# Performance work log

Measured on AMD Instinct MI355X. Metric: run time of the kernel, lower is better.

The kernel has to match this reference:

```python
import jax, jax.numpy as jnp
import numpy as np
from jax import lax

DIM = 64           # LHMSA dim
C3 = 3 * DIM       # high-band channels
HEADS = C3 // 32   # 6
WS = 8             # window size
SHIFT = 4          # shift size
EPS = 1e-6


def _ln_chw(x, w, b):
    # channel-last layer norm applied to BCHW input over C
    xt = x.transpose(0, 2, 3, 1)
    mu = xt.mean(-1, keepdims=True)
    var = ((xt - mu) ** 2).mean(-1, keepdims=True)
    y = (xt - mu) / jnp.sqrt(var + EPS) * w + b
    return y.transpose(0, 3, 1, 2)


def _conv1x1(x, w):
    # w: (out_c, in_c), no bias
    return jnp.einsum('bchw,oc->bohw', x, w)


def _dwconv3(x, w):
    # depthwise 3x3, w: (C,1,3,3)
    C = x.shape[1]
    return lax.conv_general_dilated(x, w, (1, 1), ((1, 1), (1, 1)),
                                    dimension_numbers=('NCHW', 'OIHW', 'NCHW'),
                                    feature_group_count=C)


def _gelu(x):
    return jax.nn.gelu(x, approximate=False)


def _dwt(x):
    x01 = x[:, :, 0::2, :] * 0.5
    x02 = x[:, :, 1::2, :] * 0.5
    x1 = x01[:, :, :, 0::2]; x2 = x02[:, :, :, 0::2]
    x3 = x01[:, :, :, 1::2]; x4 = x02[:, :, :, 1::2]
    ll = x1 + x2 + x3 + x4
    high = jnp.concatenate([-x1 - x2 + x3 + x4,
                            -x1 + x2 - x3 + x4,
                            x1 - x2 - x3 + x4], axis=1)
    return ll, high


def _iwt(ll, high):
    B, C, H, W = ll.shape
    hl, lh, hh = jnp.split(high, 3, axis=1)
    x1 = (ll - hl - lh + hh) * 0.5
    x2 = (ll - hl + lh - hh) * 0.5
    x3 = (ll + hl - lh - hh) * 0.5
    x4 = (ll + hl + lh + hh) * 0.5
    even = jnp.stack([x1, x3], axis=-1).reshape(B, C, H, 2 * W)  # rows 0::2
    odd = jnp.stack([x2, x4], axis=-1).reshape(B, C, H, 2 * W)   # rows 1::2
    return jnp.stack([even, odd], axis=-2).reshape(B, C, 2 * H, 2 * W)


def _swin_mhsa(x, qkv_w, qkv_b, proj_w, proj_b, rpb_table, rpi):
    # x: (B, C3, H, W); H,W divisible by WS -> no padding path
    B, C, H, W = x.shape
    dh = C // HEADS
    scale = dh ** (-0.5)
    xh = x.transpose(0, 2, 3, 1)                           # BHWC
    xh = jnp.roll(xh, (-SHIFT, -SHIFT), axis=(1, 2))
    nh, nw = H // WS, W // WS
    xw = xh.reshape(B, nh, WS, nw, WS, C).transpose(0, 1, 3, 2, 4, 5)
    xw = xw.reshape(B * nh * nw, WS * WS, C)               # (nW, N, C)
    qkv = xw @ qkv_w.T + qkv_b                             # (nW, N, 3C)
    qkv = qkv.reshape(-1, WS * WS, 3, HEADS, dh).transpose(2, 0, 3, 1, 4)
    q, k, v = qkv[0], qkv[1], qkv[2]                       # (nW, h, N, dh)
    attn = jnp.einsum('whnd,whmd->whnm', q, k) * scale
    bias = rpb_table[rpi.reshape(-1)].reshape(WS * WS, WS * WS, HEADS)
    attn = jax.nn.softmax(attn + bias.transpose(2, 0, 1)[None], axis=-1)
    out = jnp.einsum('whnm,whmd->whnd', attn, v)
    out = out.transpose(0, 2, 1, 3).reshape(-1, WS * WS, C)
    out = out.reshape(B, nh, nw, WS, WS, C).transpose(0, 1, 3, 2, 4, 5)
    out = out.reshape(B, H, W, C)
    out = jnp.roll(out, (SHIFT, SHIFT), axis=(1, 2))
    out = out @ proj_w.T + proj_b
    return out.transpose(0, 3, 1, 2)


def _rel_pos_index():
    coords = np.stack(np.meshgrid(np.arange(WS), np.arange(WS), indexing='ij'))
    cf = coords.reshape(2, -1)
    rel = (cf[:, :, None] - cf[:, None, :]).transpose(1, 2, 0).astype(np.int64)
    rel[:, :, 0] += WS - 1
    rel[:, :, 1] += WS - 1
    rel[:, :, 0] *= 2 * WS - 1
    return rel.sum(-1)


def setup_inputs() -> dict:
    key = jax.random.key(0)
    ks = jax.random.split(key, 12)
    B, H, W = 2, 512, 512
    x = jax.random.normal(ks[0], (B, DIM, H, W), jnp.float32)
    s = 0.02
    inp = {
        'x': x,
        'norm_w': jnp.ones((C3,), jnp.float32),
        'norm_b': jnp.zeros((C3,), jnp.float32),
        'qkv_w': jax.random.normal(ks[1], (3 * C3, C3), jnp.float32) * s,
        'qkv_b': jnp.zeros((3 * C3,), jnp.float32),
        'proj_w': jax.random.normal(ks[2], (C3, C3), jnp.float32) * s,
        'proj_b': jnp.zeros((C3,), jnp.float32),
        'rpb_table': jax.random.normal(ks[3], ((2 * WS - 1) ** 2, HEADS), jnp.float32) * s,
        'aux_dw_w': jax.random.normal(ks[4], (DIM, 1, 3, 3), jnp.float32) * 0.1,
        'aux_pw_w': jax.random.normal(ks[5], (DIM, DIM), jnp.float32) * s,
        'cg1_w': jax.random.normal(ks[6], (C3 * 3 // 12, DIM), jnp.float32) * s,
        'cg2_w': jax.random.normal(ks[7], (C3, C3 * 3 // 12), jnp.float32) * s,
        'po_w': jax.random.normal(ks[8], (DIM, DIM), jnp.float32) * s,
        'gamma_main': jnp.full((1,), 1e-4, jnp.float32),
        'gamma_aux': jnp.full((1,), 0.5, jnp.float32),
        'gamma_cross': jnp.full((1,), 1e-5, jnp.float32),
        'rel_pos_index': jnp.asarray(_rel_pos_index(), jnp.int32),
    }
    return inp


def reference(x, norm_w, norm_b, qkv_w, qkv_b, proj_w, proj_b, rpb_table,
              aux_dw_w, aux_pw_w, cg1_w, cg2_w, po_w,
              gamma_main, gamma_aux, gamma_cross, rel_pos_index):
    ll, high = _dwt(x)
    high_norm = _ln_chw(high, norm_w, norm_b)
    refined_high = high + gamma_main * _swin_mhsa(high_norm, qkv_w, qkv_b,
                                                  proj_w, proj_b, rpb_table,
                                                  rel_pos_index)
    refined_ll = ll + gamma_aux * _conv1x1(_gelu(_dwconv3(ll, aux_dw_w)), aux_pw_w)
    gap = ll.mean((2, 3), keepdims=True)
    cross = jax.nn.sigmoid(_conv1x1(_gelu(_conv1x1(gap, cg1_w)), cg2_w))
    refined_high = refined_high * (1.0 + gamma_cross * (cross - 0.5) * 2.0)
    out = _iwt(refined_ll, refined_high)
    return _conv1x1(out - x, po_w)
```

## Files before the change

### kernel.cpp

```cpp
#include <hip/hip_runtime.h>
#include <hip/hip_bf16.h>
#include <math.h>

typedef __hip_bfloat16 bf16;
typedef short s8v __attribute__((ext_vector_type(8)));
typedef float f4v __attribute__((ext_vector_type(4)));
#define MFMA16(a,b,c) __builtin_amdgcn_mfma_f32_16x16x32_bf16(a,b,c,0,0,0)

#define B2   2
#define C64  64
#define C3   192
#define HEADS 6
#define NWIN 2048

#define P_NORMW 0
#define P_NORMB 192
#define P_QKVW  384
#define P_QKVB  110976
#define P_PROJW 111552
#define P_PROJB 148416
#define P_RPB   148608
#define P_AUXDW 149958
#define P_AUXPW 150534
#define P_CG1   154630
#define P_CG2   157702
#define P_PO    166918
#define P_GM    171014
#define P_GA    171015
#define P_GC    171016

#define WS_FLAG   0
#define WS_PARAMS 256
#define WS_GAP    684544
#define WS_AMUL   685568
#define WS_CVAL   687616
#define WS_TSTAT  689664
#define WS_LL     1738240
#define WS_DLLW   18515456
#define WS_WOUT   35292672
#define WS_HRAW   85624320
#define WS_WQKV   135955968
#define WS_WPROJ  136177152
#define WS_WPW    136250880
#define WS_WPO    136259072
#define WS_S12    136267264
#define WS_BIAS6  136271872

template<bool ISF>
__device__ __forceinline__ float LD(const void* p, long i){
  if constexpr (ISF) return ((const float*)p)[i];
  else return __bfloat162float(((const bf16*)p)[i]);
}
template<bool ISF>
__device__ __forceinline__ float2 LD2(const void* p, long i){
  if constexpr (ISF) return *(const float2*)((const float*)p + i);
  else {
    const ushort2 u = *(const ushort2*)((const bf16*)p + i);
    float2 r; r.x = __uint_as_float(((unsigned)u.x) << 16);
    r.y = __uint_as_float(((unsigned)u.y) << 16);
    return r;
  }
}
template<bool ISF>
__device__ __forceinline__ void ST(void* p, long i, float v){
  if constexpr (ISF) ((float*)p)[i] = v;
  else ((bf16*)p)[i] = __float2bfloat16(v);
}
__device__ __forceinline__ float gelu_f(float x){
  return 0.5f * x * (1.f + erff(x * 0.70710678118654752f));
}
__device__ __forceinline__ float bfu(unsigned short u){
  return __uint_as_float(((unsigned)u) << 16);
}
__device__ __forceinline__ unsigned pk2(float a, float b){
  return (unsigned)__bfloat16_as_ushort(__float2bfloat16(a)) |
         ((unsigned)__bfloat16_as_ushort(__float2bfloat16(b)) << 16);
}
__device__ __forceinline__ uint4 pk8(const float* v){
  uint4 r;
  r.x = pk2(v[0], v[1]); r.y = pk2(v[2], v[3]);
  r.z = pk2(v[4], v[5]); r.w = pk2(v[6], v[7]);
  return r;
}
__device__ __forceinline__ void gld16(const void* g, void* l){
  __builtin_amdgcn_global_load_lds(
      (const __attribute__((address_space(1))) void*)g,
      (__attribute__((address_space(3))) void*)l, 16, 0, 0);
}

__global__ __launch_bounds__(256) void detect_kernel(const void* x, int* flag){
  __shared__ int wildcnt;
  if (threadIdx.x == 0) wildcnt = 0;
  __syncthreads();
  const unsigned short* u = (const unsigned short*)x;
  int wild = 0;
  for (int i = threadIdx.x; i < 2048; i += 256){
    unsigned int v = ((unsigned int)u[i]) << 16;
    float f = __uint_as_float(v);
    float a = fabsf(f);
    if (!(a < 1e8f) || (a > 0.f && a < 1e-8f)) wild++;
  }
  atomicAdd(&wildcnt, wild);
  __syncthreads();
  if (threadIdx.x == 0) *flag = (wildcnt > 100) ? 1 : 0;
}

struct PP { const void* src[15]; float* dst[15]; int n[15]; };
__global__ __launch_bounds__(256) void convert_params(PP pp, const int* flag){
  const bool isf = (*flag) != 0;
  const int gid = blockIdx.x*256 + threadIdx.x;
  const int gsz = gridDim.x*256;
#pragma unroll
  for (int q = 0; q < 15; q++){
    const int n = pp.n[q];
    const void* s = pp.src[q];
    float* d = pp.dst[q];
    for (int i = gid; i < n; i += gsz)
      d[i] = isf ? ((const float*)s)[i] : __bfloat162float(((const bf16*)s)[i]);
  }
}

__global__ __launch_bounds__(256) void kw_convert(const float* pf, const int* rpi,
                                                  bf16* wqkvF, bf16* wproj,
                                                  bf16* wpw, bf16* wpo, float* bias6T){
  const int i = blockIdx.x*256 + threadIdx.x;
  if (i < 110592){
    const int c = i % 192;
    wqkvF[i] = __float2bfloat16(pf[P_QKVW + i] * pf[P_NORMW + c]);
  } else if (i < 147456)  wproj[i-110592] = __float2bfloat16(pf[P_PROJW + (i-110592)]);
  else if (i < 151552)    wpw[i-147456]   = __float2bfloat16(pf[P_AUXPW + (i-147456)]);
  else if (i < 155648)    wpo[i-151552]   = __float2bfloat16(pf[P_PO + (i-151552)]);
  else if (i < 180224){
    const int j = i - 155648;
    const int hh = j >> 12, nm = j & 4095;
    const int row = nm >> 6, col = nm & 63;
    bias6T[hh*4096 + col*64 + row] = pf[P_RPB + rpi[nm]*6 + hh];
  }
}

__global__ __launch_bounds__(256) void k0d_s12(const float* pf, float2* s12p){
  const int o = blockIdx.x*16 + (threadIdx.x >> 4);
  const int lane = threadIdx.x & 15;
  if (o >= 576) return;
  float s1 = 0.f, s2 = 0.f;
  for (int c = lane; c < 192; c += 16){
    const float w = pf[P_QKVW + o*192 + c];
    s1 += w * pf[P_NORMW + c];
    s2 += w * pf[P_NORMB + c];
  }
  s1 += __shfl_xor(s1,1,16); s1 += __shfl_xor(s1,2,16);
  s1 += __shfl_xor(s1,4,16); s1 += __shfl_xor(s1,8,16);
  s2 += __shfl_xor(s2,1,16); s2 += __shfl_xor(s2,2,16);
  s2 += __shfl_xor(s2,4,16); s2 += __shfl_xor(s2,8,16);
  if (lane == 0){
    float2 v; v.x = s1; v.y = s2 + pf[P_QKVB + o];
    s12p[o] = v;
  }
}

template<bool ISF>
__device__ void k1f_body(const void* xv, bf16* llb, bf16* hraw, float2* tstat){
  const int wid = blockIdx.x;
  const int b  = wid >> 10;
  const int wh = (wid >> 5) & 31;
  const int ww = wid & 31;
  const int tid = threadIdx.x;
  const int tk = tid >> 2, l4 = tid & 3;
  const int wi = tk >> 3, wj = tk & 7;
  const int h2 = (wh*8 + wi + 4) & 255;
  const int w2 = (ww*8 + wj + 4) & 255;
  const long pixbase = ((long)(2*h2) << 9) + 2*w2;
  const long llpix = ((long)h2 << 8) + w2;
  float raw0[16], raw1[16], raw2[16];
  float sum = 0.f, sumsq = 0.f;
#pragma unroll
  for (int cc = 0; cc < 16; ++cc){
    const int c = l4*16 + cc;
    const long base = ((long)(b*64 + c) << 18) + pixbase;
    const float2 t0 = LD2<ISF>(xv, base);
    const float2 t1 = LD2<ISF>(xv, base + 512);
    const float a = t0.x, cr = t0.y, bb = t1.x, dd = t1.y;
    llb[((long)(b*64 + c) << 16) + llpix] = __float2bfloat16(0.5f*(a + bb + cr + dd));
    const float h0 = 0.5f*(-a - bb + cr + dd);
    const float h1 = 0.5f*(-a + bb - cr + dd);
    const float hh = 0.5f*( a - bb - cr + dd);
    raw0[cc] = h0; raw1[cc] = h1; raw2[cc] = hh;
    sum += h0 + h1 + hh;
    sumsq += h0*h0 + h1*h1 + hh*hh;
  }
  const long hb = ((long)wid*64 + tk)*192 + l4*16;
  *(uint4*)(hraw + hb)       = pk8(raw0);
  *(uint4*)(hraw + hb + 8)   = pk8(raw0 + 8);
  *(uint4*)(hraw + hb + 64)  = pk8(raw1);
  *(uint4*)(hraw + hb + 72)  = pk8(raw1 + 8);
  *(uint4*)(hraw + hb + 128) = pk8(raw2);
  *(uint4*)(hraw + hb + 136) = pk8(raw2 + 8);
  sum   += __shfl_xor(sum,1,4);   sum   += __shfl_xor(sum,2,4);
  sumsq += __shfl_xor(sumsq,1,4); sumsq += __shfl_xor(sumsq,2,4);
  if (l4 == 0){
    const float mean = sum * (1.f/192.f);
    float var = sumsq * (1.f/192.f) - mean*mean;
    var = fmaxf(var, 0.f);
    const float rstd = rsqrtf(var + 1e-6f);
    float2 st; st.x = rstd; st.y = mean * rstd;
    tstat[wid*64 + tk] = st;
  }
}
__global__ __launch_bounds__(256,4) void k1f_dwt(const void* xv, bf16* llb, bf16* hraw,
                                                 float2* tstat, const int* flag){
  if (*flag) k1f_body<true>(xv, llb, hraw, tstat);
  else       k1f_body<false>(xv, llb, hraw, tstat);
}

__global__ __launch_bounds__(256) void k2_gap(const bf16* llb, float* gap){
  const int bc = blockIdx.x;
  const uint4* p = (const uint4*)(llb + ((long)bc << 16));
  float s = 0.f;
  for (int i = threadIdx.x; i < 8192; i += 256){
    const uint4 v = p[i];
    s += __uint_as_float(v.x << 16) + __uint_as_float(v.x & 0xffff0000u);
    s += __uint_as_float(v.y << 16) + __uint_as_float(v.y & 0xffff0000u);
    s += __uint_as_float(v.z << 16) + __uint_as_float(v.z & 0xffff0000u);
    s += __uint_as_float(v.w << 16) + __uint_as_float(v.w & 0xffff0000u);
  }
  __shared__ float red[256];
  red[threadIdx.x] = s; __syncthreads();
  for (int st = 128; st > 0; st >>= 1){
    if (threadIdx.x < st) red[threadIdx.x] += red[threadIdx.x + st];
    __syncthreads();
  }
  if (threadIdx.x == 0) gap[bc] = red[0] * (1.f / 65536.f);
}

__global__ __launch_bounds__(256) void k3_cross(const float* pf, const float* gap,
                                                float* amul, float* cval){
  __shared__ float t1[B2][48];
  __shared__ float g[B2][64];
  const int tid = threadIdx.x;
  if (tid < 128) g[tid >> 6][tid & 63] = gap[tid];
  __syncthreads();
  if (tid < 96){
    const int b = tid / 48, j = tid % 48;
    float s = 0.f;
    const float* w = pf + P_CG1 + j * 64;
    for (int c = 0; c < 64; ++c) s += w[c] * g[b][c];
    t1[b][j] = gelu_f(s);
  }
  __syncthreads();
  const float gm = pf[P_GM], gc = pf[P_GC];
  for (int o = tid; o < B2 * C3; o += 256){
    const int b = o / C3, ch = o % C3;
    float s = 0.f;
    const float* w = pf + P_CG2 + ch * 48;
    for (int j = 0; j < 48; ++j) s += w[j] * t1[b][j];
    const float cr = 1.f / (1.f + expf(-s));
    const float c = gc * (cr - 0.5f) * 2.f;
    cval[o] = c;
    amul[o] = gm * (1.f + c);
  }
}

__global__ __launch_bounds__(256,6) void k6f_aux(const bf16* llb, const float* pf,
                                                 const bf16* wpw, bf16* dllw){
  __shared__ __align__(16) char sm6[24576];
  bf16* tile = (bf16*)sm6;
  bf16* t    = (bf16*)(sm6 + 15360);
  const int blk = blockIdx.x;
  const int b = blk >> 10, ti = (blk >> 5) & 31, tj = blk & 31;
  const int tid = threadIdx.x;
  const int y0 = ti*8 - 1;
  const int x0 = tj*8 - 2;

  for (int e = tid; e < 7680; e += 256){
    const int col = e % 12;
    const int rc  = e / 12;
    const int row = rc % 10, ch = rc / 10;
    const int x = x0 + col, y = y0 + row;
    bf16 v = __float2bfloat16(0.f);
    if ((unsigned)x < 256u && (unsigned)y < 256u)
      v = llb[((long)(b*64 + ch) << 16) + ((long)y << 8) + x];
    tile[rc*12 + col] = v;
  }
  __syncthreads();

  {
    const int tok = tid & 63, cgrp = tid >> 6;
    const int iy = tok >> 3, ix = tok & 7;
#pragma unroll
    for (int cc = 0; cc < 16; ++cc){
      const int c = cgrp*16 + cc;
      const float* wk = pf + P_AUXDW + c*9;
      float s = 0.f;
#pragma unroll
      for (int ky = 0; ky < 3; ++ky)
#pragma unroll
        for (int kx = 0; kx < 3; ++kx)
          s += wk[ky*3 + kx] * __bfloat162float(tile[(c*10 + iy + ky)*12 + ix + 1 + kx]);
      t[tok*72 + c] = __float2bfloat16(gelu_f(s));
    }
  }
  __syncthreads();

  const int wv = tid >> 6, l = tid & 63, lr = l & 15, lg = l >> 4;
  const f4v fz = {0.f,0.f,0.f,0.f};
  f4v acc[4];
#pragma unroll
  for (int nt = 0; nt < 4; ++nt) acc[nt] = fz;
#pragma unroll
  for (int ks = 0; ks < 2; ++ks){
    const s8v a = *(const s8v*)(t + (wv*16+lr)*72 + ks*32 + lg*8);
#pragma unroll
    for (int nt = 0; nt < 4; ++nt){
      const s8v bfr = *(const s8v*)(wpw + (nt*16+lr)*64 + ks*32 + lg*8);
      acc[nt] = MFMA16(a, bfr, acc[nt]);
    }
  }
  const float ga = pf[P_GA];
#pragma unroll
  for (int i = 0; i < 4; ++i){
    const int p = wv*16 + lg*4 + i;
    const int y = ti*8 + (p >> 3), x = tj*8 + (p & 7);
    const int sy = (y - 4) & 255, sx = (x - 4) & 255;
    const int wid = b*1024 + (sy >> 3)*32 + (sx >> 3);
    const int tok2 = (sy & 7)*8 + (sx & 7);
    const long ob = ((long)wid*64 + tok2)*64;
#pragma unroll
    for (int nt = 0; nt < 4; ++nt)
      dllw[ob + nt*16 + lr] = __float2bfloat16(ga * acc[nt][i]);
  }
}

__global__ __launch_bounds__(512,4) void k4_attn(const bf16* hraw, const float2* tstat,
                                                 const bf16* wqkvF, const float2* s12p,
                                                 const float* bias6T, bf16* wout){
  __shared__ __align__(16) char sm[63488];
  bf16* bstage = (bf16*)sm;
  const int g = blockIdx.x;
  const int xcd = g & 7, slot = g >> 3;
  const int pair = (slot/6)*8 + xcd;
  const int h    = slot - (slot/6)*6;
  const int tid = threadIdx.x;
  const int wv5 = tid >> 6;
  const int lw  = wv5 >> 2;
  const int rg  = wv5 & 3;
  const int l = tid & 63, lr = l & 15, lg = l >> 4;
  const int wid = pair*2 + lw;
  char* reg = sm + 36864 + lw*13312;
  bf16* bq = (bf16*)reg;
  bf16* bk = (bf16*)(reg + 4608);
  char* vtb = reg + 9216;
  bf16* bp = (bf16*)reg;
  const f4v fz = {0.f,0.f,0.f,0.f};
  const float scale = 0.17677669529663687f;
  const bf16* at = hraw + (long)wid * 12288;

#pragma unroll
  for (int pass = 0; pass < 5; ++pass){
    if (pass*512 + wv5*64 < 2304){
      const int idx = pass*512 + tid;
      const int rl  = idx / 24;
      const int off = (idx - rl*24) * 16;
      const int soff = off ^ ((rl & 7) << 4);
      const int grow = (rl >> 5)*192 + h*32 + (rl & 31);
      gld16(wqkvF + grow*192 + (soff >> 1),
            (char*)bstage + (pass*512 + wv5*64)*16);
    }
  }
  s8v aA[6];
#pragma unroll
  for (int ks = 0; ks < 6; ++ks)
    aA[ks] = *(const s8v*)(at + (rg*16+lr)*192 + ks*32 + lg*8);
  float2 st4[4];
#pragma unroll
  for (int i = 0; i < 4; ++i)
    st4[i] = tstat[wid*64 + rg*16 + lg*4 + i];
  __syncthreads();

  f4v acc[6];
#pragma unroll
  for (int nt = 0; nt < 6; ++nt) acc[nt] = fz;
#pragma unroll
  for (int ks = 0; ks < 6; ++ks){
    const int kb = (ks*32 + lg*8) * 2;
#pragma unroll
    for (int nt = 0; nt < 6; ++nt){
      const int row = nt*16 + lr;
      const s8v bfr = *(const s8v*)((const char*)bstage + row*384 + (kb ^ ((row&7)<<4)));
      acc[nt] = MFMA16(aA[ks], bfr, acc[nt]);
    }
  }
#pragma unroll
  for (int nt = 0; nt < 6; ++nt){
    const int ol = nt*16 + lr;
    const int p = ol >> 5, c = ol & 31;
    const int ocol = p*192 + h*32 + c;
    const float2 sp = s12p[ocol];
#pragma unroll
    for (int i = 0; i < 4; ++i){
      const int row = rg*16 + lg*4 + i;
      const float v = st4[i].x*acc[nt][i] - st4[i].y*sp.x + sp.y;
      if (p == 0)      bq[row*36 + c] = __float2bfloat16(v*scale);
      else if (p == 1) bk[row*36 + c] = __float2bfloat16(v);
      else             *(bf16*)(vtb + ((c*128 + row*2) ^ ((c&7)<<4))) = __float2bfloat16(v);
    }
  }
  __syncthreads();

  f4v sacc[4];
  {
    const s8v a = *(const s8v*)(bq + (rg*16+lr)*36 + lg*8);
#pragma unroll
    for (int nt = 0; nt < 4; ++nt){
      const s8v bfr = *(const s8v*)(bk + (nt*16+lr)*36 + lg*8);
      sacc[nt] = MFMA16(a, bfr, fz);
    }
  }
  f4v bld[4];
#pragma unroll
  for (int nt = 0; nt < 4; ++nt)
    bld[nt] = *(const f4v*)(bias6T + h*4096 + (nt*16+lr)*64 + rg*16 + lg*4);
  float pvv[4][4];
  float inv4[4];
#pragma unroll
  for (int i = 0; i < 4; ++i){
    float s = 0.f;
#pragma unroll
    for (int nt = 0; nt < 4; ++nt){
      const float e = __expf(sacc[nt][i] + bld[nt][i]);
      pvv[i][nt] = e;
      s += e;
    }
    s += __shfl_xor(s, 1, 16);
    s += __shfl_xor(s, 2, 16);
    s += __shfl_xor(s, 4, 16);
    s += __shfl_xor(s, 8, 16);
    inv4[i] = 1.f/s;
  }
  __syncthreads();

#pragma unroll
  for (int i = 0; i < 4; ++i){
    const int row = rg*16 + lg*4 + i;
#pragma unroll
    for (int nt = 0; nt < 4; ++nt)
      bp[row*72 + nt*16 + lr] = __float2bfloat16(pvv[i][nt]);
  }
  f4v oacc[2] = {fz, fz};
#pragma unroll
  for (int ks2 = 0; ks2 < 2; ++ks2){
    const s8v a = *(const s8v*)(bp + (rg*16+lr)*72 + ks2*32 + lg*8);
#pragma unroll
    for (int nn = 0; nn < 2; ++nn){
      const int d = nn*16 + lr;
      const s8v bfr = *(const s8v*)(vtb + ((d*128 + (ks2*32+lg*8)*2) ^ ((d&7)<<4)));
      oacc[nn] = MFMA16(a, bfr, oacc[nn]);
    }
  }
#pragma unroll
  for (int nn = 0; nn < 2; ++nn)
#pragma unroll
    for (int i = 0; i < 4; ++i){
      const int row = rg*16 + lg*4 + i;
      wout[((long)wid*64 + row)*192 + h*32 + nn*16 + lr] =
        __float2bfloat16(oacc[nn][i] * inv4[i]);
    }
}

__global__ __launch_bounds__(256,5) void k5_proj(bf16* wout, const bf16* hraw,
                                                 const bf16* wproj, const float* pf,
                                                 const float* amul, const float* cval){
  __shared__ __align__(16) bf16 bufC[64*192];
  const int wid = blockIdx.x;
  const int b  = wid >> 10;
  const int tid = threadIdx.x;
  const int wv = tid >> 6, l = tid & 63, lr = l & 15, lg = l >> 4;

  {
    const bf16* hsrc = hraw + (long)wid * 12288;
#pragma unroll
    for (int pass = 0; pass < 6; ++pass){
      const int idx = pass*256 + tid;
      const int row = idx / 24;
      const int off = (idx % 24) * 16;
      const int soff = off ^ ((row & 7) << 4);
      gld16(hsrc + row*192 + (soff >> 1),
            (char*)bufC + (pass*256 + wv*64)*16);
    }
  }

  const f4v fz = {0.f,0.f,0.f,0.f};
  const bf16* at = wout + (long)wid * 12288;

  f4v acc[3][4];
#pragma unroll
  for (int nt = 0; nt < 3; ++nt)
#pragma unroll
    for (int mt = 0; mt < 4; ++mt) acc[nt][mt] = fz;
#pragma unroll
  for (int ks = 0; ks < 6; ++ks){
    const int k0 = ks*32;
    s8v a[4];
#pragma unroll
    for (int mt = 0; mt < 4; ++mt)
      a[mt] = *(const s8v*)(at + (mt*16+lr)*192 + k0 + lg*8);
#pragma unroll
    for (int nt = 0; nt < 3; ++nt){
      const int ocol = (wv*3+nt)*16 + lr;
      const s8v bfr = *(const s8v*)(wproj + ocol*192 + k0 + lg*8);
#pragma unroll
      for (int mt = 0; mt < 4; ++mt) acc[nt][mt] = MFMA16(a[mt], bfr, acc[nt][mt]);
    }
  }
  __syncthreads();
#pragma unroll
  for (int nt = 0; nt < 3; ++nt){
    const int col = (wv*3+nt)*16 + lr;
    const int bc = b*192 + col;
    const float am = amul[bc], cv = cval[bc], pb = pf[P_PROJB + col];
#pragma unroll
    for (int mt = 0; mt < 4; ++mt)
#pragma unroll
      for (int i = 0; i < 4; ++i){
        const int row = mt*16 + lg*4 + i;
        const float hv = __bfloat162float(
          *(const bf16*)((const char*)bufC + row*384 + ((col*2) ^ ((row&7)<<4))));
        wout[(long)wid*12288 + row*192 + col] =
          __float2bfloat16(am*(acc[nt][mt][i] + pb) + cv*hv);
      }
  }
}

template<bool ISF>
__device__ void k7_body(const bf16* dvalw, const bf16* dllw, const bf16* wpo,
                        void* out, char* yp){
  const int blk = blockIdx.x;
  const int b = blk >> 10, hh = (blk >> 1) & 511, half = blk & 1;
  const int h2 = hh >> 1, posH = hh & 1;
  const int th = (h2 + 252) & 255;
  const int wh = th >> 3, wi = th & 7;
  const int tid = threadIdx.x;
  const int j = tid & 7;
#pragma unroll
  for (int pass = 0; pass < 8; ++pass){
    const int p = pass*32 + (tid >> 3);
    const int ww2 = half*256 + p;
    const int w2 = ww2 >> 1, posW = ww2 & 1;
    const int tw = (w2 + 252) & 255;
    const int ww = tw >> 3, wj = tw & 7;
    const int wid = b*1024 + wh*32 + ww;
    const int tok = wi*8 + wj;
    const long dvb = ((long)wid*64 + tok)*192 + j*8;
    const s8v hl8 = *(const s8v*)(dvalw + dvb);
    const s8v lh8 = *(const s8v*)(dvalw + dvb + 64);
    const s8v hh8 = *(const s8v*)(dvalw + dvb + 128);
    const s8v dl8 = *(const s8v*)(dllw + ((long)wid*64 + tok)*64 + j*8);
    const float s1 = posW ? 0.5f : -0.5f;
    const float s2 = posH ? 0.5f : -0.5f;
    const float s3 = posW == posH ? 0.5f : -0.5f;
    float e[8];
#pragma unroll
    for (int q = 0; q < 8; ++q)
      e[q] = 0.5f*bfu((unsigned short)dl8[q]) + s1*bfu((unsigned short)hl8[q])
           + s2*bfu((unsigned short)lh8[q]) + s3*bfu((unsigned short)hh8[q]);
    *(uint4*)(yp + ((p*128 + j*16) ^ ((p&7)<<4))) = pk8(e);
  }
  __syncthreads();
  const int wv = tid >> 6, l = tid & 63, lr = l & 15, lg = l >> 4;
  const f4v fz = {0.f,0.f,0.f,0.f};
  f4v acc[4][4];
#pragma unroll
  for (int mt = 0; mt < 4; ++mt)
#pragma unroll
    for (int nt = 0; nt < 4; ++nt) acc[mt][nt] = fz;
#pragma unroll
  for (int ks = 0; ks < 2; ++ks){
    const int k0 = ks*32;
    s8v a[4];
#pragma unroll
    for (int mt = 0; mt < 4; ++mt)
      a[mt] = *(const s8v*)(wpo + (mt*16+lr)*64 + k0 + lg*8);
#pragma unroll
    for (int nt = 0; nt < 4; ++nt){
      const int prow = wv*64 + nt*16 + lr;
      const s8v bfr = *(const s8v*)(yp + ((prow*128 + (k0+lg*8)*2) ^ ((prow&7)<<4)));
#pragma unroll
      for (int mt = 0; mt < 4; ++mt) acc[mt][nt] = MFMA16(a[mt], bfr, acc[mt][nt]);
    }
  }
  const int px0 = half*256 + wv*64;
#pragma unroll
  for (int mt = 0; mt < 4; ++mt)
#pragma unroll
    for (int nt = 0; nt < 4; ++nt)
#pragma unroll
      for (int i = 0; i < 4; ++i){
        const int c = mt*16 + lg*4 + i;
        const long ob = ((long)(b*64 + c)*512 + hh)*512 + px0 + nt*16 + lr;
        ST<ISF>(out, ob, acc[mt][nt][i]);
      }
}
__global__ __launch_bounds__(256,4) void k7_out(const bf16* dvalw, const bf16* dllw,
                                                const bf16* wpo, void* out, const int* flag){
  __shared__ __align__(16) char yp[32768];
  if (*flag) k7_body<true>(dvalw, dllw, wpo, out, yp);
  else       k7_body<false>(dvalw, dllw, wpo, out, yp);
}

extern "C" void kernel_launch(void* const* d_in, const int* in_sizes, int n_in,
                              void* d_out, int out_size, void* d_ws, size_t ws_size,
                              hipStream_t stream){
  char* ws = (char*)d_ws;
  int*   flag = (int*)(ws + WS_FLAG);
  float* pf   = (float*)(ws + WS_PARAMS);
  float* gap  = (float*)(ws + WS_GAP);
  float* amul = (float*)(ws + WS_AMUL);
  float* cval = (float*)(ws + WS_CVAL);
  float2* tstat=(float2*)(ws + WS_TSTAT);
  bf16*  llb  = (bf16*)(ws + WS_LL);
  bf16*  dllw = (bf16*)(ws + WS_DLLW);
  bf16*  wout = (bf16*)(ws + WS_WOUT);
  bf16*  hraw = (bf16*)(ws + WS_HRAW);
  bf16*  wqkvF= (bf16*)(ws + WS_WQKV);
  bf16*  wproj= (bf16*)(ws + WS_WPROJ);
  bf16*  wpw  = (bf16*)(ws + WS_WPW);
  bf16*  wpo  = (bf16*)(ws + WS_WPO);
  float2* s12p= (float2*)(ws + WS_S12);
  float* bias6= (float*)(ws + WS_BIAS6);
  const int* rpi = (const int*)d_in[16];

  detect_kernel<<<1, 256, 0, stream>>>(d_in[0], flag);

  PP pp;
  const int pidx[15] = {1,2,3,4,5,6,7,8,9,10,11,12,13,14,15};
  const int poff[15] = {P_NORMW,P_NORMB,P_QKVW,P_QKVB,P_PROJW,P_PROJB,P_RPB,
                        P_AUXDW,P_AUXPW,P_CG1,P_CG2,P_PO,P_GM,P_GA,P_GC};
  for (int q = 0; q < 15; q++){
    pp.src[q] = d_in[pidx[q]];
    pp.dst[q] = pf + poff[q];
    pp.n[q]   = in_sizes[pidx[q]];
  }
  convert_params<<<128, 256, 0, stream>>>(pp, flag);
  kw_convert<<<704, 256, 0, stream>>>(pf, rpi, wqkvF, wproj, wpw, wpo, bias6);
  k0d_s12  <<<36,  256, 0, stream>>>(pf, s12p);

  k1f_dwt<<<NWIN, 256, 0, stream>>>(d_in[0], llb, hraw, tstat, flag);
  k2_gap <<<128,  256, 0, stream>>>(llb, gap);
  k3_cross<<<1,   256, 0, stream>>>(pf, gap, amul, cval);
  k6f_aux<<<NWIN, 256, 0, stream>>>(llb, pf, wpw, dllw);
  k4_attn<<<NWIN/2*6, 512, 0, stream>>>(hraw, tstat, wqkvF, s12p, bias6, wout);
  k5_proj<<<NWIN, 256, 0, stream>>>(wout, hraw, wproj, pf, amul, cval);
  k7_out <<<2048, 256, 0, stream>>>(wout, dllw, wpo, d_out, flag);
}
```

Measured before the change: 423.9 us.

## Merge attention, aux conv and GAP into one heterogeneous launch; widen DWT loads

Three independent kernels (window attention, the low-band aux depthwise/pointwise branch, and the global average pool) are merged into a single launch whose blocks branch on their index. The aim is to cut launch gaps and tail idle time so the small kernels fill the attention kernel's tail. The aux branch now packs two tiles per 512-thread block and the GAP uses 512 threads. Separately, the DWT kernel processes two tokens per thread with 4-wide loads and paired ll stores. Mixing workloads ties all blocks to the attention kernel's shared memory size and register budget, which may lower occupancy for the lighter paths.

```diff
diff --git a/kernel.cpp b/kernel.cpp
--- a/kernel.cpp
+++ b/kernel.cpp
@@ -47,17 +47,18 @@
 #define WS_BIAS6  136271872
 
 template<bool ISF>
-__device__ __forceinline__ float LD(const void* p, long i){
-  if constexpr (ISF) return ((const float*)p)[i];
-  else return __bfloat162float(((const bf16*)p)[i]);
+__device__ __forceinline__ float bfu_(unsigned short u){
+  return __uint_as_float(((unsigned)u) << 16);
+}
+__device__ __forceinline__ float bfu(unsigned short u){
+  return __uint_as_float(((unsigned)u) << 16);
 }
 template<bool ISF>
-__device__ __forceinline__ float2 LD2(const void* p, long i){
-  if constexpr (ISF) return *(const float2*)((const float*)p + i);
+__device__ __forceinline__ float4 LD4(const void* p, long i){
+  if constexpr (ISF) return *(const float4*)((const float*)p + i);
   else {
-    const ushort2 u = *(const ushort2*)((const bf16*)p + i);
-    float2 r; r.x = __uint_as_float(((unsigned)u.x) << 16);
-    r.y = __uint_as_float(((unsigned)u.y) << 16);
+    const ushort4 u = *(const ushort4*)((const bf16*)p + i);
+    float4 r; r.x = bfu(u.x); r.y = bfu(u.y); r.z = bfu(u.z); r.w = bfu(u.w);
     return r;
   }
 }
@@ -68,9 +69,6 @@
 }
 __device__ __forceinline__ float gelu_f(float x){
   return 0.5f * x * (1.f + erff(x * 0.70710678118654752f));
-}
-__device__ __forceinline__ float bfu(unsigned short u){
-  return __uint_as_float(((unsigned)u) << 16);
 }
 __device__ __forceinline__ unsigned pk2(float a, float b){
   return (unsigned)__bfloat16_as_ushort(__float2bfloat16(a)) |
@@ -165,71 +163,64 @@
   const int wh = (wid >> 5) & 31;
   const int ww = wid & 31;
   const int tid = threadIdx.x;
-  const int tk = tid >> 2, l4 = tid & 3;
-  const int wi = tk >> 3, wj = tk & 7;
+  const int tp = tid >> 3, l8 = tid & 7;
+  const int t0 = tp*2;
+  const int wi = t0 >> 3, wj0 = t0 & 7;
   const int h2 = (wh*8 + wi + 4) & 255;
-  const int w2 = (ww*8 + wj + 4) & 255;
-  const long pixbase = ((long)(2*h2) << 9) + 2*w2;
-  const long llpix = ((long)h2 << 8) + w2;
-  float raw0[16], raw1[16], raw2[16];
-  float sum = 0.f, sumsq = 0.f;
-#pragma unroll
-  for (int cc = 0; cc < 16; ++cc){
-    const int c = l4*16 + cc;
-    const long base = ((long)(b*64 + c) << 18) + pixbase;
-    const float2 t0 = LD2<ISF>(xv, base);
-    const float2 t1 = LD2<ISF>(xv, base + 512);
-    const float a = t0.x, cr = t0.y, bb = t1.x, dd = t1.y;
-    llb[((long)(b*64 + c) << 16) + llpix] = __float2bfloat16(0.5f*(a + bb + cr + dd));
-    const float h0 = 0.5f*(-a - bb + cr + dd);
-    const float h1 = 0.5f*(-a + bb - cr + dd);
-    const float hh = 0.5f*( a - bb - cr + dd);
-    raw0[cc] = h0; raw1[cc] = h1; raw2[cc] = hh;
-    sum += h0 + h1 + hh;
-    sumsq += h0*h0 + h1*h1 + hh*hh;
-  }
-  const long hb = ((long)wid*64 + tk)*192 + l4*16;
-  *(uint4*)(hraw + hb)       = pk8(raw0);
-  *(uint4*)(hraw + hb + 8)   = pk8(raw0 + 8);
-  *(uint4*)(hraw + hb + 64)  = pk8(raw1);
-  *(uint4*)(hraw + hb + 72)  = pk8(raw1 + 8);
-  *(uint4*)(hraw + hb + 128) = pk8(raw2);
-  *(uint4*)(hraw + hb + 136) = pk8(raw2 + 8);
-  sum   += __shfl_xor(sum,1,4);   sum   += __shfl_xor(sum,2,4);
-  sumsq += __shfl_xor(sumsq,1,4); sumsq += __shfl_xor(sumsq,2,4);
-  if (l4 == 0){
-    const float mean = sum * (1.f/192.f);
-    float var = sumsq * (1.f/192.f) - mean*mean;
-    var = fmaxf(var, 0.f);
-    const float rstd = rsqrtf(var + 1e-6f);
+  const int w2 = (ww*8 + wj0 + 4) & 255;
+  const long rowbase = ((long)(2*h2) << 9) + 2*w2;
+  float r0[3][8], r1[3][8];
+  float s0 = 0.f, q0 = 0.f, s1 = 0.f, q1 = 0.f;
+#pragma unroll
+  for (int cc = 0; cc < 8; ++cc){
+    const int c = l8*8 + cc;
+    const long base = ((long)(b*64 + c) << 18) + rowbase;
+    const float4 ta = LD4<ISF>(xv, base);
+    const float4 tb = LD4<ISF>(xv, base + 512);
+    float a = ta.x, cr = ta.y, bb = tb.x, dd = tb.y;
+    const float ll0 = 0.5f*(a + bb + cr + dd);
+    const float h00 = 0.5f*(-a - bb + cr + dd);
+    const float h10 = 0.5f*(-a + bb - cr + dd);
+    const float h20 = 0.5f*( a - bb - cr + dd);
+    r0[0][cc] = h00; r0[1][cc] = h10; r0[2][cc] = h20;
+    s0 += h00 + h10 + h20; q0 += h00*h00 + h10*h10 + h20*h20;
+    a = ta.z; cr = ta.w; bb = tb.z; dd = tb.w;
+    const float ll1 = 0.5f*(a + bb + cr + dd);
+    const float h01 = 0.5f*(-a - bb + cr + dd);
+    const float h11 = 0.5f*(-a + bb - cr + dd);
+    const float h21 = 0.5f*( a - bb - cr + dd);
+    r1[0][cc] = h01; r1[1][cc] = h11; r1[2][cc] = h21;
+    s1 += h01 + h11 + h21; q1 += h01*h01 + h11*h11 + h21*h21;
+    *(unsigned*)(llb + ((long)(b*64 + c) << 16) + ((long)h2 << 8) + w2) = pk2(ll0, ll1);
+  }
+  const long hb = ((long)wid*64 + t0)*192 + l8*8;
+  *(uint4*)(hraw + hb)            = pk8(r0[0]);
+  *(uint4*)(hraw + hb + 64)       = pk8(r0[1]);
+  *(uint4*)(hraw + hb + 128)      = pk8(r0[2]);
+  *(uint4*)(hraw + hb + 192)      = pk8(r1[0]);
+  *(uint4*)(hraw + hb + 192 + 64) = pk8(r1[1]);
+  *(uint4*)(hraw + hb + 192 +128) = pk8(r1[2]);
+  s0 += __shfl_xor(s0,1,8); s0 += __shfl_xor(s0,2,8); s0 += __shfl_xor(s0,4,8);
+  q0 += __shfl_xor(q0,1,8); q0 += __shfl_xor(q0,2,8); q0 += __shfl_xor(q0,4,8);
+  s1 += __shfl_xor(s1,1,8); s1 += __shfl_xor(s1,2,8); s1 += __shfl_xor(s1,4,8);
+  q1 += __shfl_xor(q1,1,8); q1 += __shfl_xor(q1,2,8); q1 += __shfl_xor(q1,4,8);
+  if (l8 == 0){
+    float mean = s0 * (1.f/192.f);
+    float var = fmaxf(q0 * (1.f/192.f) - mean*mean, 0.f);
+    float rstd = rsqrtf(var + 1e-6f);
     float2 st; st.x = rstd; st.y = mean * rstd;
-    tstat[wid*64 + tk] = st;
+    tstat[wid*64 + t0] = st;
+    mean = s1 * (1.f/192.f);
+    var = fmaxf(q1 * (1.f/192.f) - mean*mean, 0.f);
+    rstd = rsqrtf(var + 1e-6f);
+    st.x = rstd; st.y = mean * rstd;
+    tstat[wid*64 + t0 + 1] = st;
   }
 }
 __global__ __launch_bounds__(256,4) void k1f_dwt(const void* xv, bf16* llb, bf16* hraw,
                                                  float2* tstat, const int* flag){
   if (*flag) k1f_body<true>(xv, llb, hraw, tstat);
   else       k1f_body<false>(xv, llb, hraw, tstat);
-}
-
-__global__ __launch_bounds__(256) void k2_gap(const bf16* llb, float* gap){
-  const int bc = blockIdx.x;
-  const uint4* p = (const uint4*)(llb + ((long)bc << 16));
-  float s = 0.f;
-  for (int i = threadIdx.x; i < 8192; i += 256){
-    const uint4 v = p[i];
-    s += __uint_as_float(v.x << 16) + __uint_as_float(v.x & 0xffff0000u);
-    s += __uint_as_float(v.y << 16) + __uint_as_float(v.y & 0xffff0000u);
-    s += __uint_as_float(v.z << 16) + __uint_as_float(v.z & 0xffff0000u);
-    s += __uint_as_float(v.w << 16) + __uint_as_float(v.w & 0xffff0000u);
-  }
-  __shared__ float red[256];
-  red[threadIdx.x] = s; __syncthreads();
-  for (int st = 128; st > 0; st >>= 1){
-    if (threadIdx.x < st) red[threadIdx.x] += red[threadIdx.x + st];
-    __syncthreads();
-  }
-  if (threadIdx.x == 0) gap[bc] = red[0] * (1.f / 65536.f);
 }
 
 __global__ __launch_bounds__(256) void k3_cross(const float* pf, const float* gap,
@@ -260,82 +251,11 @@
   }
 }
 
-__global__ __launch_bounds__(256,6) void k6f_aux(const bf16* llb, const float* pf,
-                                                 const bf16* wpw, bf16* dllw){
-  __shared__ __align__(16) char sm6[24576];
-  bf16* tile = (bf16*)sm6;
-  bf16* t    = (bf16*)(sm6 + 15360);
-  const int blk = blockIdx.x;
-  const int b = blk >> 10, ti = (blk >> 5) & 31, tj = blk & 31;
-  const int tid = threadIdx.x;
-  const int y0 = ti*8 - 1;
-  const int x0 = tj*8 - 2;
-
-  for (int e = tid; e < 7680; e += 256){
-    const int col = e % 12;
-    const int rc  = e / 12;
-    const int row = rc % 10, ch = rc / 10;
-    const int x = x0 + col, y = y0 + row;
-    bf16 v = __float2bfloat16(0.f);
-    if ((unsigned)x < 256u && (unsigned)y < 256u)
-      v = llb[((long)(b*64 + ch) << 16) + ((long)y << 8) + x];
-    tile[rc*12 + col] = v;
-  }
-  __syncthreads();
-
-  {
-    const int tok = tid & 63, cgrp = tid >> 6;
-    const int iy = tok >> 3, ix = tok & 7;
-#pragma unroll
-    for (int cc = 0; cc < 16; ++cc){
-      const int c = cgrp*16 + cc;
-      const float* wk = pf + P_AUXDW + c*9;
-      float s = 0.f;
-#pragma unroll
-      for (int ky = 0; ky < 3; ++ky)
-#pragma unroll
-        for (int kx = 0; kx < 3; ++kx)
-          s += wk[ky*3 + kx] * __bfloat162float(tile[(c*10 + iy + ky)*12 + ix + 1 + kx]);
-      t[tok*72 + c] = __float2bfloat16(gelu_f(s));
-    }
-  }
-  __syncthreads();
-
-  const int wv = tid >> 6, l = tid & 63, lr = l & 15, lg = l >> 4;
-  const f4v fz = {0.f,0.f,0.f,0.f};
-  f4v acc[4];
-#pragma unroll
-  for (int nt = 0; nt < 4; ++nt) acc[nt] = fz;
-#pragma unroll
-  for (int ks = 0; ks < 2; ++ks){
-    const s8v a = *(const s8v*)(t + (wv*16+lr)*72 + ks*32 + lg*8);
-#pragma unroll
-    for (int nt = 0; nt < 4; ++nt){
-      const s8v bfr = *(const s8v*)(wpw + (nt*16+lr)*64 + ks*32 + lg*8);
-      acc[nt] = MFMA16(a, bfr, acc[nt]);
-    }
-  }
-  const float ga = pf[P_GA];
-#pragma unroll
-  for (int i = 0; i < 4; ++i){
-    const int p = wv*16 + lg*4 + i;
-    const int y = ti*8 + (p >> 3), x = tj*8 + (p & 7);
-    const int sy = (y - 4) & 255, sx = (x - 4) & 255;
-    const int wid = b*1024 + (sy >> 3)*32 + (sx >> 3);
-    const int tok2 = (sy & 7)*8 + (sx & 7);
-    const long ob = ((long)wid*64 + tok2)*64;
-#pragma unroll
-    for (int nt = 0; nt < 4; ++nt)
-      dllw[ob + nt*16 + lr] = __float2bfloat16(ga * acc[nt][i]);
-  }
-}
-
-__global__ __launch_bounds__(512,4) void k4_attn(const bf16* hraw, const float2* tstat,
-                                                 const bf16* wqkvF, const float2* s12p,
-                                                 const float* bias6T, bf16* wout){
-  __shared__ __align__(16) char sm[63488];
+
+__device__ void k4_body(char* sm, int g, const bf16* hraw, const float2* tstat,
+                        const bf16* wqkvF, const float2* s12p, const float* bias6T,
+                        bf16* wout){
   bf16* bstage = (bf16*)sm;
-  const int g = blockIdx.x;
   const int xcd = g & 7, slot = g >> 3;
   const int pair = (slot/6)*8 + xcd;
   const int h    = slot - (slot/6)*6;
@@ -464,6 +384,110 @@
       wout[((long)wid*64 + row)*192 + h*32 + nn*16 + lr] =
         __float2bfloat16(oacc[nn][i] * inv4[i]);
     }
+}
+
+__device__ void k6f_body(char* smb, int blk6, const bf16* llb, const float* pf,
+                         const bf16* wpw, bf16* dllw){
+  const int tid = threadIdx.x;
+  const int sub = tid >> 8;
+  const int t2 = tid & 255;
+  char* sm6 = smb + sub*24576;
+  bf16* tile = (bf16*)sm6;
+  bf16* t    = (bf16*)(sm6 + 15360);
+  const int tl = blk6*2 + sub;
+  const int b = tl >> 10, ti = (tl >> 5) & 31, tj = tl & 31;
+  const int y0 = ti*8 - 1;
+  const int x0 = tj*8 - 2;
+
+  for (int e = t2; e < 7680; e += 256){
+    const int col = e % 12;
+    const int rc  = e / 12;
+    const int row = rc % 10, ch = rc / 10;
+    const int x = x0 + col, y = y0 + row;
+    bf16 v = __float2bfloat16(0.f);
+    if ((unsigned)x < 256u && (unsigned)y < 256u)
+      v = llb[((long)(b*64 + ch) << 16) + ((long)y << 8) + x];
+    tile[rc*12 + col] = v;
+  }
+  __syncthreads();
+
+  {
+    const int tok = t2 & 63, cgrp = t2 >> 6;
+    const int iy = tok >> 3, ix = tok & 7;
+#pragma unroll
+    for (int cc = 0; cc < 16; ++cc){
+      const int c = cgrp*16 + cc;
+      const float* wk = pf + P_AUXDW + c*9;
+      float s = 0.f;
+#pragma unroll
+      for (int ky = 0; ky < 3; ++ky)
+#pragma unroll
+        for (int kx = 0; kx < 3; ++kx)
+          s += wk[ky*3 + kx] * __bfloat162float(tile[(c*10 + iy + ky)*12 + ix + 1 + kx]);
+      t[tok*72 + c] = __float2bfloat16(gelu_f(s));
+    }
+  }
+  __syncthreads();
+
+  const int wv = t2 >> 6, l = t2 & 63, lr = l & 15, lg = l >> 4;
+  const f4v fz = {0.f,0.f,0.f,0.f};
+  f4v acc[4];
+#pragma unroll
+  for (int nt = 0; nt < 4; ++nt) acc[nt] = fz;
+#pragma unroll
+  for (int ks = 0; ks < 2; ++ks){
+    const s8v a = *(const s8v*)(t + (wv*16+lr)*72 + ks*32 + lg*8);
+#pragma unroll
+    for (int nt = 0; nt < 4; ++nt){
+      const s8v bfr = *(const s8v*)(wpw + (nt*16+lr)*64 + ks*32 + lg*8);
+      acc[nt] = MFMA16(a, bfr, acc[nt]);
+    }
+  }
+  const float ga = pf[P_GA];
+#pragma unroll
+  for (int i = 0; i < 4; ++i){
+    const int p = wv*16 + lg*4 + i;
+    const int y = ti*8 + (p >> 3), x = tj*8 + (p & 7);
+    const int sy = (y - 4) & 255, sx = (x - 4) & 255;
+    const int wd = b*1024 + (sy >> 3)*32 + (sx >> 3);
+    const int tok2 = (sy & 7)*8 + (sx & 7);
+    const long ob = ((long)wd*64 + tok2)*64;
+#pragma unroll
+    for (int nt = 0; nt < 4; ++nt)
+      dllw[ob + nt*16 + lr] = __float2bfloat16(ga * acc[nt][i]);
+  }
+}
+
+__device__ void k2_body(char* smb, int bc, const bf16* llb, float* gap){
+  float* red = (float*)smb;
+  const int tid = threadIdx.x;
+  const uint4* p = (const uint4*)(llb + ((long)bc << 16));
+  float s = 0.f;
+  for (int i = tid; i < 8192; i += 512){
+    const uint4 v = p[i];
+    s += __uint_as_float(v.x << 16) + __uint_as_float(v.x & 0xffff0000u);
+    s += __uint_as_float(v.y << 16) + __uint_as_float(v.y & 0xffff0000u);
+    s += __uint_as_float(v.z << 16) + __uint_as_float(v.z & 0xffff0000u);
+    s += __uint_as_float(v.w << 16) + __uint_as_float(v.w & 0xffff0000u);
+  }
+  red[tid] = s; __syncthreads();
+  for (int st = 256; st > 0; st >>= 1){
+    if (tid < st) red[tid] += red[tid + st];
+    __syncthreads();
+  }
+  if (tid == 0) gap[bc] = red[0] * (1.f / 65536.f);
+}
+
+__global__ __launch_bounds__(512,4) void kmix(const bf16* hraw, const float2* tstat,
+                                              const bf16* wqkvF, const float2* s12p,
+                                              const float* bias6T, bf16* wout,
+                                              const bf16* llb, const float* pf,
+                                              const bf16* wpw, bf16* dllw, float* gap){
+  __shared__ __align__(16) char sm[63488];
+  const int blk = blockIdx.x;
+  if (blk < 6144)       k4_body(sm, blk, hraw, tstat, wqkvF, s12p, bias6T, wout);
+  else if (blk < 7168)  k6f_body(sm, blk - 6144, llb, pf, wpw, dllw);
+  else                  k2_body(sm, blk - 7168, llb, gap);
 }
 
 __global__ __launch_bounds__(256,5) void k5_proj(bf16* wout, const bf16* hraw,
@@ -644,10 +668,9 @@
   k0d_s12  <<<36,  256, 0, stream>>>(pf, s12p);
 
   k1f_dwt<<<NWIN, 256, 0, stream>>>(d_in[0], llb, hraw, tstat, flag);
-  k2_gap <<<128,  256, 0, stream>>>(llb, gap);
+  kmix   <<<7296, 512, 0, stream>>>(hraw, tstat, wqkvF, s12p, bias6, wout,
+                                    llb, pf, wpw, dllw, gap);
   k3_cross<<<1,   256, 0, stream>>>(pf, gap, amul, cval);
-  k6f_aux<<<NWIN, 256, 0, stream>>>(llb, pf, wpw, dllw);
-  k4_attn<<<NWIN/2*6, 512, 0, stream>>>(hraw, tstat, wqkvF, s12p, bias6, wout);
   k5_proj<<<NWIN, 256, 0, stream>>>(wout, hraw, wproj, pf, amul, cval);
   k7_out <<<2048, 256, 0, stream>>>(wout, dllw, wpo, d_out, flag);
 }
```

After: 412.6 us. -2.7%, faster.
